# Kernel optimization log

Measured on AMD Instinct MI355X. Metric: run time of the kernel, lower is better.

## Reference

```python
import jax, jax.numpy as jnp
import numpy as np

TEMPERATURE = 0.05


def _hungarian_max(C):
    """Jonker-Volgenant shortest-augmenting-path LAP on a square numpy matrix.
    Returns col index matched to each row, maximizing total cost
    (equivalent to scipy.optimize.linear_sum_assignment(C, maximize=True))."""
    cost = -np.asarray(C, dtype=np.float64)  # minimize negated cost
    n = cost.shape[0]
    INF = np.inf
    u = np.zeros(n + 1)
    v = np.zeros(n + 1)
    p = np.zeros(n + 1, dtype=np.int64)   # p[j] = row matched to column j (1-based)
    way = np.zeros(n + 1, dtype=np.int64)
    for i in range(1, n + 1):
        p[0] = i
        j0 = 0
        minv = np.full(n + 1, INF)
        used = np.zeros(n + 1, dtype=bool)
        while True:
            used[j0] = True
            i0 = p[j0]
            delta = INF
            j1 = -1
            for j in range(1, n + 1):
                if not used[j]:
                    cur = cost[i0 - 1, j - 1] - u[i0] - v[j]
                    if cur < minv[j]:
                        minv[j] = cur
                        way[j] = j0
                    if minv[j] < delta:
                        delta = minv[j]
                        j1 = j
            for j in range(n + 1):
                if used[j]:
                    u[p[j]] += delta
                    v[j] -= delta
                else:
                    minv[j] -= delta
            j0 = j1
            if p[j0] == 0:
                break
        while j0:
            j1 = way[j0]
            p[j0] = p[j1]
            j0 = j1
    col_of_row = np.zeros(n, dtype=np.int64)
    for j in range(1, n + 1):
        col_of_row[p[j] - 1] = j - 1
    return col_of_row


def setup_inputs() -> dict:
    key = jax.random.key(0)
    k1, k2, k3 = jax.random.split(key, 3)
    B, K, D = 256, 16, 1024
    return {
        "outputs": jax.random.normal(k1, (B, K, D), dtype=jnp.float32),
        "positive_embeddings": jax.random.normal(k2, (B, K, D), dtype=jnp.float32),
        "negative_embeddings": jax.random.normal(k3, (B, K, D), dtype=jnp.float32),
    }


def reference(outputs, positive_embeddings, negative_embeddings):
    B, K, D = outputs.shape
    o = outputs.reshape(B * K, D) / TEMPERATURE          # (BK, D)
    emb = jnp.concatenate(
        [positive_embeddings.reshape(B * K, D),
         negative_embeddings.reshape(B * K, D)], axis=0)  # (2BK, D)
    sim = jnp.einsum("bd,cd->bc", o, emb)                 # (BK, 2BK)
    sim = jax.nn.log_softmax(sim, axis=1)
    # i-th KxK diagonal block: rows [K*i, K*(i+1)), cols [K*i, K*(i+1))
    idx = jnp.arange(B)
    blocks = sim.reshape(B, K, 2 * B, K)[idx, :, idx, :]  # (B, K, K)
    # Hungarian matching (detached in original -> no grad through assignment)
    blk_np = np.asarray(jax.device_get(jax.lax.stop_gradient(blocks)))
    cols = jnp.asarray(np.stack([_hungarian_max(blk_np[b]) for b in range(B)]))  # (B, K)
    matched = blocks[idx[:, None], jnp.arange(K)[None, :], cols]  # (B, K)
    # per-sample mean of -matched, then mean over batch == overall mean
    return jnp.mean(-matched)
```

## Files before the change

kernel.cpp:

```cpp
#include <hip/hip_runtime.h>
#include <hip/hip_bf16.h>
#include <math.h>

#define Ddim 1024
#define Mrows 4096
#define Ncols 8192
#define BM 128
#define BN 128
#define BK 32
#define NCS 64
#define CS 128
#define RT (Mrows / BM)
#define KITERS (Ddim / BK)
#define SCALE 20.0f
#define ARR_ELEMS (Mrows * Ddim)

typedef __bf16 bf16_t;
typedef __bf16 bf16x8 __attribute__((ext_vector_type(8)));
typedef float f32x4 __attribute__((ext_vector_type(4)));

#define LOAD16_TO_LDS(g, l)                                                  \
  __builtin_amdgcn_global_load_lds(                                          \
      (const __attribute__((address_space(1))) void*)(g),                    \
      (__attribute__((address_space(3))) void*)(l), 16, 0, 0)

__global__ __launch_bounds__(256) void cvt_kernel(
    const float* __restrict__ o, const float* __restrict__ pos,
    const float* __restrict__ neg, bf16_t* __restrict__ ob,
    bf16_t* __restrict__ pb, bf16_t* __restrict__ nb)
{
  const int idx = blockIdx.x * 256 + threadIdx.x;
  const int seg = idx >> 19;
  const int off = idx & ((1 << 19) - 1);
  const float* src = (seg == 0) ? o : (seg == 1) ? pos : neg;
  bf16_t* dst = (seg == 0) ? ob : (seg == 1) ? pb : nb;
  const float4 v0 = *(const float4*)(src + (size_t)off * 8);
  const float4 v1 = *(const float4*)(src + (size_t)off * 8 + 4);
  bf16x8 r = {(bf16_t)v0.x, (bf16_t)v0.y, (bf16_t)v0.z, (bf16_t)v0.w,
              (bf16_t)v1.x, (bf16_t)v1.y, (bf16_t)v1.z, (bf16_t)v1.w};
  *(bf16x8*)(dst + (size_t)off * 8) = r;
}

__global__ __launch_bounds__(256, 4) void gemm_lse_kernel(
    const bf16_t* __restrict__ ob, const bf16_t* __restrict__ pb,
    const bf16_t* __restrict__ nb, float* __restrict__ pm,
    float* __restrict__ pl, float* __restrict__ blocks_raw)
{
  __shared__ bf16_t As[2][BM * BK];
  __shared__ bf16_t Bs[2][BN * BK];

  const int bid = blockIdx.x;
  const int rt = bid >> 6;
  const int cs = bid & 63;
  const int row0 = rt * BM;
  const bf16_t* Eb = (cs < 32) ? (pb + (size_t)cs * BN * Ddim)
                               : (nb + (size_t)(cs - 32) * BN * Ddim);

  const int t = threadIdx.x;
  const int wave = t >> 6;
  const int wr = wave & 1;
  const int wc = wave >> 1;
  const int lane = t & 63;
  const int quad = lane >> 4;
  const int l16 = lane & 15;
  const int koff = ((quad ^ ((l16 >> 1) & 3)) << 3);
  const int lr4 = lane >> 2;
  const int cstg = lane & 3;

  f32x4 acc[4][4];
#pragma unroll
  for (int a = 0; a < 4; ++a)
#pragma unroll
    for (int b = 0; b < 4; ++b) acc[a][b] = (f32x4){0.f, 0.f, 0.f, 0.f};

#pragma unroll
  for (int cl = 0; cl < 2; ++cl) {
    const int r = wave * 32 + cl * 16 + lr4;
    const int gc = cstg ^ ((r >> 1) & 3);
    LOAD16_TO_LDS(ob + (size_t)(row0 + r) * Ddim + gc * 8,
                  &As[0][(wave * 32 + cl * 16) * BK]);
    LOAD16_TO_LDS(Eb + (size_t)r * Ddim + gc * 8,
                  &Bs[0][(wave * 32 + cl * 16) * BK]);
  }

  int p = 0;
  for (int kc = 0; kc < KITERS; ++kc) {
    __syncthreads();
    if (kc + 1 < KITERS) {
      const int k0 = (kc + 1) * BK;
#pragma unroll
      for (int cl = 0; cl < 2; ++cl) {
        const int r = wave * 32 + cl * 16 + lr4;
        const int gc = cstg ^ ((r >> 1) & 3);
        LOAD16_TO_LDS(ob + (size_t)(row0 + r) * Ddim + k0 + gc * 8,
                      &As[p ^ 1][(wave * 32 + cl * 16) * BK]);
        LOAD16_TO_LDS(Eb + (size_t)r * Ddim + k0 + gc * 8,
                      &Bs[p ^ 1][(wave * 32 + cl * 16) * BK]);
      }
    }

    bf16x8 af[4];
#pragma unroll
    for (int fm = 0; fm < 4; ++fm)
      af[fm] = *(const bf16x8*)(&As[p][(wr * 64 + fm * 16 + l16) * BK + koff]);
#pragma unroll
    for (int fn = 0; fn < 4; ++fn) {
      const bf16x8 bf = *(const bf16x8*)(&Bs[p][(wc * 64 + fn * 16 + l16) * BK + koff]);
#pragma unroll
      for (int fm = 0; fm < 4; ++fm)
        acc[fm][fn] = __builtin_amdgcn_mfma_f32_16x16x32_bf16(af[fm], bf, acc[fm][fn], 0, 0, 0);
    }
    p ^= 1;
  }

  const int csp = cs * 2 + wc;
#pragma unroll
  for (int fm = 0; fm < 4; ++fm) {
#pragma unroll
    for (int r = 0; r < 4; ++r) {
      float s[4];
#pragma unroll
      for (int fn = 0; fn < 4; ++fn) s[fn] = acc[fm][fn][r] * SCALE;
      float m = fmaxf(fmaxf(s[0], s[1]), fmaxf(s[2], s[3]));
#pragma unroll
      for (int off = 1; off <= 8; off <<= 1)
        m = fmaxf(m, __shfl_xor(m, off, 64));
      float l = 0.f;
#pragma unroll
      for (int fn = 0; fn < 4; ++fn) l += __expf(s[fn] - m);
#pragma unroll
      for (int off = 1; off <= 8; off <<= 1)
        l += __shfl_xor(l, off, 64);
      if (l16 == 0) {
        const int rg = row0 + wr * 64 + fm * 16 + quad * 4 + r;
        pm[(size_t)rg * CS + csp] = m;
        pl[(size_t)rg * CS + csp] = l;
      }
    }
  }

  if (cs == rt && wr == wc) {
#pragma unroll
    for (int fm = 0; fm < 4; ++fm) {
      const int b = rt * 8 + wr * 4 + fm;
#pragma unroll
      for (int r = 0; r < 4; ++r)
        blocks_raw[b * 256 + (quad * 4 + r) * 16 + l16] = acc[fm][fm][r] * SCALE;
    }
  }
}

__global__ __launch_bounds__(64) void hungarian_kernel(
    const float* __restrict__ blocks_raw, const float* __restrict__ pm,
    const float* __restrict__ pl, float* __restrict__ out)
{
  const int b = blockIdx.x;
  const int L = threadIdx.x;
  __shared__ float C[16][16];
  __shared__ float lse_s[16];

  for (int e = L; e < 256; e += 64)
    C[e >> 4][e & 15] = blocks_raw[b * 256 + e];

  {
    const int r = L & 15, g = L >> 4;
    const size_t base = (size_t)(b * 16 + r) * CS + g * 32;
    float m = -INFINITY, l = 0.f;
#pragma unroll
    for (int k = 0; k < 32; ++k) {
      const float m2 = pm[base + k];
      const float l2 = pl[base + k];
      const float M = fmaxf(m, m2);
      l = l * __expf(m - M) + l2 * __expf(m2 - M);
      m = M;
    }
#pragma unroll
    for (int off = 16; off <= 32; off <<= 1) {
      const float m2 = __shfl_xor(m, off, 64);
      const float l2 = __shfl_xor(l, off, 64);
      const float M = fmaxf(m, m2);
      l = l * __expf(m - M) + l2 * __expf(m2 - M);
      m = M;
    }
    if (g == 0) lse_s[r] = m + logf(l);
  }

  const float INF = 3.0e38f;
  float vj = 0.f, u_reg = 0.f;
  int pj = 0;
  float minv = INF;
  int wayj = 0;
  bool usedj = false, on_tree = false;

  for (int i = 1; i <= 16; ++i) {
    if (L == 0) pj = i;
    minv = INF; wayj = 0; usedj = false; on_tree = false;
    int j0 = 0;
    while (true) {
      usedj = usedj || (L == j0);
      const int i0 = __shfl(pj, j0, 64);
      if (L == i0) on_tree = true;
      const float ui0 = __shfl(u_reg, i0, 64);
      if (L >= 1 && L <= 16 && !usedj) {
        const float cur = -C[i0 - 1][L - 1] - ui0 - vj;
        if (cur < minv) { minv = cur; wayj = j0; }
      }
      float cand = (L >= 1 && L <= 16 && !usedj) ? minv : INF;
      int idx = L;
#pragma unroll
      for (int off = 16; off > 0; off >>= 1) {
        const float ov = __shfl_xor(cand, off, 32);
        const int oi = __shfl_xor(idx, off, 32);
        if (ov < cand || (ov == cand && oi < idx)) { cand = ov; idx = oi; }
      }
      const float delta = cand;
      const int j1 = __builtin_amdgcn_readfirstlane(idx);
      if (L >= 1 && L <= 16) {
        if (usedj) vj -= delta; else minv -= delta;
        if (on_tree) u_reg += delta;
      }
      j0 = j1;
      const int pj0 = __shfl(pj, j0, 64);
      if (pj0 == 0) break;
    }
    while (j0 != 0) {
      const int j1a = __shfl(wayj, j0, 64);
      const int pjn = __shfl(pj, j1a, 64);
      if (L == j0) pj = pjn;
      j0 = j1a;
    }
  }

  float loss = 0.f;
  if (L >= 1 && L <= 16) loss = lse_s[pj - 1] - C[pj - 1][L - 1];
#pragma unroll
  for (int off = 32; off > 0; off >>= 1) loss += __shfl_down(loss, off, 64);
  if (L == 0) atomicAdd(out, loss * (1.0f / 4096.0f));
}

extern "C" void kernel_launch(void* const* d_in, const int* in_sizes, int n_in,
                              void* d_out, int out_size, void* d_ws, size_t ws_size,
                              hipStream_t stream) {
  const float* o   = (const float*)d_in[0];
  const float* pos = (const float*)d_in[1];
  const float* neg = (const float*)d_in[2];
  float* out = (float*)d_out;

  float* ws = (float*)d_ws;
  float* pm         = ws;
  float* pl         = pm + (size_t)4096 * CS;
  float* blocks_raw = pl + (size_t)4096 * CS;
  bf16_t* ob = (bf16_t*)(blocks_raw + 65536);
  bf16_t* pb = ob + (size_t)ARR_ELEMS;
  bf16_t* nb = pb + (size_t)ARR_ELEMS;

  hipMemsetAsync(out, 0, sizeof(float), stream);
  cvt_kernel<<<3 * ARR_ELEMS / 8 / 256, 256, 0, stream>>>(o, pos, neg, ob, pb, nb);
  gemm_lse_kernel<<<RT * NCS, 256, 0, stream>>>(ob, pb, nb, pm, pl, blocks_raw);
  hungarian_kernel<<<256, 64, 0, stream>>>(blocks_raw, pm, pl, out);
}
```

Measured before the change: 225.5 us.

## Switch GEMM to FP8 e4m3 with 32x32x64 scaled MFMA

Converts inputs to FP8 e4m3 instead of bf16 and runs the similarity GEMM with the gfx950 scaled 32x32x64 f8f6f4 MFMA and unit scales. K tile grows to 64 bytes per row, and the LSE epilogue and diagonal-block extraction are remapped to the 32x32 accumulator layout. This halves global and LDS traffic and doubles MFMA throughput per byte, at the cost of much lower precision in logits scaled by 20, which could change the Hungarian assignments and the loss.

```diff
diff --git a/kernel.cpp b/kernel.cpp
--- a/kernel.cpp
+++ b/kernel.cpp
@@ -1,5 +1,6 @@
 #include <hip/hip_runtime.h>
 #include <hip/hip_bf16.h>
+#include <hip/hip_fp8.h>
 #include <math.h>
 
 #define Ddim 1024
@@ -7,17 +8,17 @@
 #define Ncols 8192
 #define BM 128
 #define BN 128
-#define BK 32
+#define BKB 64
 #define NCS 64
 #define CS 128
 #define RT (Mrows / BM)
-#define KITERS (Ddim / BK)
+#define KITERS (Ddim / BKB)
 #define SCALE 20.0f
 #define ARR_ELEMS (Mrows * Ddim)
 
-typedef __bf16 bf16_t;
-typedef __bf16 bf16x8 __attribute__((ext_vector_type(8)));
-typedef float f32x4 __attribute__((ext_vector_type(4)));
+typedef float f32x16 __attribute__((ext_vector_type(16)));
+typedef int i32x4 __attribute__((ext_vector_type(4)));
+typedef int i32x8 __attribute__((ext_vector_type(8)));
 
 #define LOAD16_TO_LDS(g, l)                                                  \
   __builtin_amdgcn_global_load_lds(                                          \
@@ -26,113 +27,137 @@
 
 __global__ __launch_bounds__(256) void cvt_kernel(
     const float* __restrict__ o, const float* __restrict__ pos,
-    const float* __restrict__ neg, bf16_t* __restrict__ ob,
-    bf16_t* __restrict__ pb, bf16_t* __restrict__ nb)
+    const float* __restrict__ neg, unsigned char* __restrict__ ob,
+    unsigned char* __restrict__ pb, unsigned char* __restrict__ nb)
 {
   const int idx = blockIdx.x * 256 + threadIdx.x;
   const int seg = idx >> 19;
   const int off = idx & ((1 << 19) - 1);
   const float* src = (seg == 0) ? o : (seg == 1) ? pos : neg;
-  bf16_t* dst = (seg == 0) ? ob : (seg == 1) ? pb : nb;
+  unsigned char* dst = (seg == 0) ? ob : (seg == 1) ? pb : nb;
   const float4 v0 = *(const float4*)(src + (size_t)off * 8);
   const float4 v1 = *(const float4*)(src + (size_t)off * 8 + 4);
-  bf16x8 r = {(bf16_t)v0.x, (bf16_t)v0.y, (bf16_t)v0.z, (bf16_t)v0.w,
-              (bf16_t)v1.x, (bf16_t)v1.y, (bf16_t)v1.z, (bf16_t)v1.w};
-  *(bf16x8*)(dst + (size_t)off * 8) = r;
+  union { unsigned char b[8]; uint2 u; } pk;
+  pk.b[0] = __hip_fp8_e4m3(v0.x).__x;
+  pk.b[1] = __hip_fp8_e4m3(v0.y).__x;
+  pk.b[2] = __hip_fp8_e4m3(v0.z).__x;
+  pk.b[3] = __hip_fp8_e4m3(v0.w).__x;
+  pk.b[4] = __hip_fp8_e4m3(v1.x).__x;
+  pk.b[5] = __hip_fp8_e4m3(v1.y).__x;
+  pk.b[6] = __hip_fp8_e4m3(v1.z).__x;
+  pk.b[7] = __hip_fp8_e4m3(v1.w).__x;
+  *(uint2*)(dst + (size_t)off * 8) = pk.u;
 }
 
 __global__ __launch_bounds__(256, 4) void gemm_lse_kernel(
-    const bf16_t* __restrict__ ob, const bf16_t* __restrict__ pb,
-    const bf16_t* __restrict__ nb, float* __restrict__ pm,
+    const unsigned char* __restrict__ ob, const unsigned char* __restrict__ pb,
+    const unsigned char* __restrict__ nb, float* __restrict__ pm,
     float* __restrict__ pl, float* __restrict__ blocks_raw)
 {
-  __shared__ bf16_t As[2][BM * BK];
-  __shared__ bf16_t Bs[2][BN * BK];
+  __shared__ unsigned char As[2][BM * BKB];
+  __shared__ unsigned char Bs[2][BN * BKB];
 
   const int bid = blockIdx.x;
   const int rt = bid >> 6;
   const int cs = bid & 63;
   const int row0 = rt * BM;
-  const bf16_t* Eb = (cs < 32) ? (pb + (size_t)cs * BN * Ddim)
-                               : (nb + (size_t)(cs - 32) * BN * Ddim);
+  const unsigned char* Eb = (cs < 32)
+      ? (pb + (size_t)cs * BN * Ddim)
+      : (nb + (size_t)(cs - 32) * BN * Ddim);
 
   const int t = threadIdx.x;
   const int wave = t >> 6;
   const int wr = wave & 1;
   const int wc = wave >> 1;
   const int lane = t & 63;
-  const int quad = lane >> 4;
-  const int l16 = lane & 15;
-  const int koff = ((quad ^ ((l16 >> 1) & 3)) << 3);
-  const int lr4 = lane >> 2;
+  const int h = lane >> 5;
+  const int r31 = lane & 31;
+  const int rstg = wave * 32 + (lane >> 2);
   const int cstg = lane & 3;
 
-  f32x4 acc[4][4];
-#pragma unroll
-  for (int a = 0; a < 4; ++a)
-#pragma unroll
-    for (int b = 0; b < 4; ++b) acc[a][b] = (f32x4){0.f, 0.f, 0.f, 0.f};
+  const int gfrag = (r31 >> 1) & 3;
+  const int c0 = (2 * h) ^ gfrag;
+  const int c1 = (2 * h + 1) ^ gfrag;
+
+  f32x16 acc[2][2];
+#pragma unroll
+  for (int a = 0; a < 2; ++a)
+#pragma unroll
+    for (int b = 0; b < 2; ++b)
+#pragma unroll
+      for (int e = 0; e < 16; ++e) acc[a][b][e] = 0.f;
 
 #pragma unroll
   for (int cl = 0; cl < 2; ++cl) {
-    const int r = wave * 32 + cl * 16 + lr4;
+    const int r = rstg + cl * 16;
     const int gc = cstg ^ ((r >> 1) & 3);
-    LOAD16_TO_LDS(ob + (size_t)(row0 + r) * Ddim + gc * 8,
-                  &As[0][(wave * 32 + cl * 16) * BK]);
-    LOAD16_TO_LDS(Eb + (size_t)r * Ddim + gc * 8,
-                  &Bs[0][(wave * 32 + cl * 16) * BK]);
+    LOAD16_TO_LDS(ob + (size_t)(row0 + r) * Ddim + gc * 16,
+                  &As[0][(wave * 32 + cl * 16) * BKB]);
+    LOAD16_TO_LDS(Eb + (size_t)r * Ddim + gc * 16,
+                  &Bs[0][(wave * 32 + cl * 16) * BKB]);
   }
 
   int p = 0;
   for (int kc = 0; kc < KITERS; ++kc) {
     __syncthreads();
     if (kc + 1 < KITERS) {
-      const int k0 = (kc + 1) * BK;
+      const int k0 = (kc + 1) * BKB;
 #pragma unroll
       for (int cl = 0; cl < 2; ++cl) {
-        const int r = wave * 32 + cl * 16 + lr4;
+        const int r = rstg + cl * 16;
         const int gc = cstg ^ ((r >> 1) & 3);
-        LOAD16_TO_LDS(ob + (size_t)(row0 + r) * Ddim + k0 + gc * 8,
-                      &As[p ^ 1][(wave * 32 + cl * 16) * BK]);
-        LOAD16_TO_LDS(Eb + (size_t)r * Ddim + k0 + gc * 8,
-                      &Bs[p ^ 1][(wave * 32 + cl * 16) * BK]);
-      }
-    }
-
-    bf16x8 af[4];
-#pragma unroll
-    for (int fm = 0; fm < 4; ++fm)
-      af[fm] = *(const bf16x8*)(&As[p][(wr * 64 + fm * 16 + l16) * BK + koff]);
-#pragma unroll
-    for (int fn = 0; fn < 4; ++fn) {
-      const bf16x8 bf = *(const bf16x8*)(&Bs[p][(wc * 64 + fn * 16 + l16) * BK + koff]);
-#pragma unroll
-      for (int fm = 0; fm < 4; ++fm)
-        acc[fm][fn] = __builtin_amdgcn_mfma_f32_16x16x32_bf16(af[fm], bf, acc[fm][fn], 0, 0, 0);
-    }
+        LOAD16_TO_LDS(ob + (size_t)(row0 + r) * Ddim + k0 + gc * 16,
+                      &As[p ^ 1][(wave * 32 + cl * 16) * BKB]);
+        LOAD16_TO_LDS(Eb + (size_t)r * Ddim + k0 + gc * 16,
+                      &Bs[p ^ 1][(wave * 32 + cl * 16) * BKB]);
+      }
+    }
+
+    i32x8 af[2], bf[2];
+#pragma unroll
+    for (int fm = 0; fm < 2; ++fm) {
+      const unsigned char* base = &As[p][(wr * 64 + fm * 32 + r31) * BKB];
+      const i32x4 lo = *(const i32x4*)(base + c0 * 16);
+      const i32x4 hi = *(const i32x4*)(base + c1 * 16);
+      af[fm][0] = lo[0]; af[fm][1] = lo[1]; af[fm][2] = lo[2]; af[fm][3] = lo[3];
+      af[fm][4] = hi[0]; af[fm][5] = hi[1]; af[fm][6] = hi[2]; af[fm][7] = hi[3];
+    }
+#pragma unroll
+    for (int fn = 0; fn < 2; ++fn) {
+      const unsigned char* base = &Bs[p][(wc * 64 + fn * 32 + r31) * BKB];
+      const i32x4 lo = *(const i32x4*)(base + c0 * 16);
+      const i32x4 hi = *(const i32x4*)(base + c1 * 16);
+      bf[fn][0] = lo[0]; bf[fn][1] = lo[1]; bf[fn][2] = lo[2]; bf[fn][3] = lo[3];
+      bf[fn][4] = hi[0]; bf[fn][5] = hi[1]; bf[fn][6] = hi[2]; bf[fn][7] = hi[3];
+    }
+#pragma unroll
+    for (int fn = 0; fn < 2; ++fn)
+#pragma unroll
+      for (int fm = 0; fm < 2; ++fm)
+        acc[fm][fn] = __builtin_amdgcn_mfma_scale_f32_32x32x64_f8f6f4(
+            af[fm], bf[fn], acc[fm][fn], 0, 0,
+            0, 0x7F7F7F7F, 0, 0x7F7F7F7F);
     p ^= 1;
   }
 
   const int csp = cs * 2 + wc;
 #pragma unroll
-  for (int fm = 0; fm < 4; ++fm) {
-#pragma unroll
-    for (int r = 0; r < 4; ++r) {
-      float s[4];
-#pragma unroll
-      for (int fn = 0; fn < 4; ++fn) s[fn] = acc[fm][fn][r] * SCALE;
-      float m = fmaxf(fmaxf(s[0], s[1]), fmaxf(s[2], s[3]));
-#pragma unroll
-      for (int off = 1; off <= 8; off <<= 1)
+  for (int fm = 0; fm < 2; ++fm) {
+#pragma unroll
+    for (int reg = 0; reg < 16; ++reg) {
+      const float s0 = acc[fm][0][reg] * SCALE;
+      const float s1 = acc[fm][1][reg] * SCALE;
+      float m = fmaxf(s0, s1);
+#pragma unroll
+      for (int off = 1; off <= 16; off <<= 1)
         m = fmaxf(m, __shfl_xor(m, off, 64));
-      float l = 0.f;
-#pragma unroll
-      for (int fn = 0; fn < 4; ++fn) l += __expf(s[fn] - m);
-#pragma unroll
-      for (int off = 1; off <= 8; off <<= 1)
+      float l = __expf(s0 - m) + __expf(s1 - m);
+#pragma unroll
+      for (int off = 1; off <= 16; off <<= 1)
         l += __shfl_xor(l, off, 64);
-      if (l16 == 0) {
-        const int rg = row0 + wr * 64 + fm * 16 + quad * 4 + r;
+      if (r31 == 0) {
+        const int rg = row0 + wr * 64 + fm * 32 +
+                       (reg & 3) + 8 * (reg >> 2) + 4 * h;
         pm[(size_t)rg * CS + csp] = m;
         pl[(size_t)rg * CS + csp] = l;
       }
@@ -141,11 +166,17 @@
 
   if (cs == rt && wr == wc) {
 #pragma unroll
-    for (int fm = 0; fm < 4; ++fm) {
-      const int b = rt * 8 + wr * 4 + fm;
-#pragma unroll
-      for (int r = 0; r < 4; ++r)
-        blocks_raw[b * 256 + (quad * 4 + r) * 16 + l16] = acc[fm][fm][r] * SCALE;
+    for (int fm = 0; fm < 2; ++fm) {
+#pragma unroll
+      for (int reg = 0; reg < 16; ++reg) {
+        const int r16 = reg >> 3;
+        if (((lane >> 4) & 1) == r16) {
+          const int bb = rt * 8 + wr * 4 + fm * 2 + r16;
+          const int row_in = (reg & 3) + 8 * ((reg >> 2) & 1) + 4 * h;
+          blocks_raw[bb * 256 + row_in * 16 + (lane & 15)] =
+              acc[fm][fm][reg] * SCALE;
+        }
+      }
     }
   }
 }
@@ -250,9 +281,9 @@
   float* pm         = ws;
   float* pl         = pm + (size_t)4096 * CS;
   float* blocks_raw = pl + (size_t)4096 * CS;
-  bf16_t* ob = (bf16_t*)(blocks_raw + 65536);
-  bf16_t* pb = ob + (size_t)ARR_ELEMS;
-  bf16_t* nb = pb + (size_t)ARR_ELEMS;
+  unsigned char* ob = (unsigned char*)(blocks_raw + 65536);
+  unsigned char* pb = ob + (size_t)ARR_ELEMS;
+  unsigned char* nb = pb + (size_t)ARR_ELEMS;
 
   hipMemsetAsync(out, 0, sizeof(float), stream);
   cvt_kernel<<<3 * ARR_ELEMS / 8 / 256, 256, 0, stream>>>(o, pos, neg, ob, pb, nb);
```

New measurement: 482.2 us. 2.14x slower.
